# Kernel tuning notes

Measured on AMD Instinct MI355X. Metric: run time of the kernel, lower is better.

The kernel has to match this reference:

```python
import jax, jax.numpy as jnp
import numpy as np

N_NODES = 512
STATE_DIM = 32
MESSAGE_DIM = 32
H_MSG = 64
H_RO = 64
N_STEPS = 5


def setup_inputs() -> dict:
    key = jax.random.key(0)
    ks = jax.random.split(key, 20)
    s = 0.01  # torch init: normal(0, 0.01) weights, zero biases
    d, m = STATE_DIM, MESSAGE_DIM
    inp = {
        "J": jax.random.normal(ks[0], (N_NODES, N_NODES), jnp.float32),
        "b": jax.random.normal(ks[1], (N_NODES,), jnp.float32),
        # message-passing MLP
        "mp_W1": jax.random.normal(ks[2], (H_MSG, 2 * d + 3), jnp.float32) * s,
        "mp_b1": jnp.zeros((H_MSG,), jnp.float32),
        "mp_W2": jax.random.normal(ks[3], (H_MSG, H_MSG), jnp.float32) * s,
        "mp_b2": jnp.zeros((H_MSG,), jnp.float32),
        "mp_W3": jax.random.normal(ks[4], (m, H_MSG), jnp.float32) * s,
        "mp_b3": jnp.zeros((m,), jnp.float32),
        # GRU (input = state_dim + message_dim, hidden = state_dim); gate order r,z,n
        "gru_Wih": jax.random.normal(ks[5], (3 * d, d + m), jnp.float32) * 0.1,
        "gru_Whh": jax.random.normal(ks[6], (3 * d, d), jnp.float32) * 0.1,
        "gru_bih": jax.random.normal(ks[7], (3 * d,), jnp.float32) * 0.1,
        "gru_bhh": jax.random.normal(ks[8], (3 * d,), jnp.float32) * 0.1,
        # readout MLP
        "r_W1": jax.random.normal(ks[9], (H_RO, d), jnp.float32) * s,
        "r_b1": jnp.zeros((H_RO,), jnp.float32),
        "r_W2": jax.random.normal(ks[10], (H_RO, H_RO), jnp.float32) * s,
        "r_b2": jnp.zeros((H_RO,), jnp.float32),
        "r_W3": jax.random.normal(ks[11], (2, H_RO), jnp.float32) * s,
        "r_b3": jnp.zeros((2,), jnp.float32),
    }
    return inp


def reference(J, b, mp_W1, mp_b1, mp_W2, mp_b2, mp_W3, mp_b3,
              gru_Wih, gru_Whh, gru_bih, gru_bhh,
              r_W1, r_b1, r_W2, r_b2, r_W3, r_b3):
    n = J.shape[0]
    d = gru_Whh.shape[1]
    # split first message-layer weight by input segments to avoid building [n,n,2d+3]
    Wi, Wj = mp_W1[:, :d], mp_W1[:, d:2 * d]          # [H, d]
    wJ, wbi, wbj = mp_W1[:, 2 * d], mp_W1[:, 2 * d + 1], mp_W1[:, 2 * d + 2]  # [H]

    def step(h, _):
        # pre[i, j, :] = W1 @ cat(h_i, h_j, J_ij, b_i, b_j) + b1
        pre = ((h @ Wi.T)[:, None, :] + (h @ Wj.T)[None, :, :]
               + J[:, :, None] * wJ + b[:, None, None] * wbi
               + b[None, :, None] * wbj + mp_b1)          # [n, n, H]
        m1 = jax.nn.relu(pre)
        m2 = jax.nn.relu(m1 @ mp_W2.T + mp_b2)            # [n, n, H]
        msg = jax.nn.relu(m2 @ mp_W3.T + mp_b3)           # [n, n, M]
        msg_sum = msg.sum(axis=0)                         # sum over senders i -> [n, M]
        # GRU cell over all nodes (torch GRU, gate order r,z,n)
        x = jnp.concatenate([h, msg_sum], axis=-1)        # [n, d+M]
        gi = x @ gru_Wih.T + gru_bih                      # [n, 3d]
        gh = h @ gru_Whh.T + gru_bhh                      # [n, 3d]
        i_r, i_z, i_n = jnp.split(gi, 3, axis=-1)
        h_r, h_z, h_n = jnp.split(gh, 3, axis=-1)
        r = jax.nn.sigmoid(i_r + h_r)
        z = jax.nn.sigmoid(i_z + h_z)
        n_g = jnp.tanh(i_n + r * h_n)
        h_new = (1.0 - z) * n_g + z * h
        return h_new, None

    h0 = jnp.zeros((n, d), J.dtype)
    h, _ = jax.lax.scan(step, h0, None, length=N_STEPS)
    y = jax.nn.relu(h @ r_W1.T + r_b1)
    y = jax.nn.relu(y @ r_W2.T + r_b2)
    y = jax.nn.relu(y @ r_W3.T + r_b3)                    # [n, 2]
    return jax.nn.sigmoid(y)
```

## Files before the change

kernel.cpp:

```cpp
#include <hip/hip_runtime.h>
#include <math.h>

#define NN 512
#define SD 32
#define HM 64
#define NB 256
#define NGRP 16

typedef __bf16 bf16x8 __attribute__((ext_vector_type(8)));
typedef float floatx4 __attribute__((ext_vector_type(4)));

struct KParams {
    const float *J, *b, *mpW1, *mpb1, *mpW2, *mpb2, *mpW3, *mpb3;
    const float *Wih, *Whh, *bih, *bhh;
    const float *rW1, *rb1, *rW2, *rb2, *rW3, *rb3;
    float *out;
    float *hb0, *hb1;
    unsigned *bar;
};

__device__ __forceinline__ float sigmoidf_(float x) {
    return 1.0f / (1.0f + __expf(-x));
}

__device__ __forceinline__ unsigned ld_bypass_u32(const unsigned* p) {
    unsigned r;
    asm volatile("global_load_dword %0, %1, off sc0 sc1\n\ts_waitcnt vmcnt(0)"
                 : "=v"(r) : "v"(p) : "memory");
    return r;
}
__device__ __forceinline__ void issue4(const float* base,
        floatx4& a, floatx4& b, floatx4& c, floatx4& d) {
    asm volatile(
        "global_load_dwordx4 %0, %4, off sc0 sc1\n\t"
        "global_load_dwordx4 %1, %4, off offset:16 sc0 sc1\n\t"
        "global_load_dwordx4 %2, %4, off offset:128 sc0 sc1\n\t"
        "global_load_dwordx4 %3, %4, off offset:144 sc0 sc1"
        : "=&v"(a), "=&v"(b), "=&v"(c), "=&v"(d) : "v"(base));
}
__device__ __forceinline__ void wait4_8(floatx4& a, floatx4& b, floatx4& c, floatx4& d) {
    asm volatile("s_waitcnt vmcnt(8)" : "+v"(a), "+v"(b), "+v"(c), "+v"(d));
}
__device__ __forceinline__ void wait4_4(floatx4& a, floatx4& b, floatx4& c, floatx4& d) {
    asm volatile("s_waitcnt vmcnt(4)" : "+v"(a), "+v"(b), "+v"(c), "+v"(d));
}
__device__ __forceinline__ void wait4_0(floatx4& a, floatx4& b, floatx4& c, floatx4& d) {
    asm volatile("s_waitcnt vmcnt(0)" : "+v"(a), "+v"(b), "+v"(c), "+v"(d));
}

__device__ __forceinline__ void xbarrier(unsigned* bar, unsigned round, int bid) {
    __syncthreads();
    if (threadIdx.x == 0) {
        unsigned g = (unsigned)bid >> 4;
        unsigned old = atomicAdd(&bar[g * 16], 1u);
        if (old + 1u == round * NGRP) {
            unsigned r2 = atomicAdd(&bar[256], 1u);
            if (r2 + 1u == round * NGRP) {
                atomicMax(&bar[272], round);
            } else {
                while (ld_bypass_u32(&bar[272]) < round) __builtin_amdgcn_s_sleep(2);
            }
        } else {
            while (ld_bypass_u32(&bar[272]) < round) __builtin_amdgcn_s_sleep(2);
        }
    }
    __syncthreads();
}

__global__ __launch_bounds__(512, 2) void fused_kernel(KParams p)
{
    __shared__ __align__(16) float m2f[8][16][68];
    __shared__ float msum[8][32];
    __shared__ float hjpS[2][64];
    __shared__ float hS[2][32];
    __shared__ float msgS[2][32];
    __shared__ float giS[2][96], ghS[2][96];

    const int tid  = threadIdx.x;
    const int lane = tid & 63;
    const int wave = tid >> 6;
    const int nsel = wave >> 2;
    const int nw   = wave & 3;
    const int j    = blockIdx.x * 2 + nsel;
    const int q    = lane >> 4;
    const int c    = lane & 15;

    if (tid < 128) {
        int node = tid >> 6, cc = tid & 63;
        int jj = blockIdx.x * 2 + node;
        const float* wr = p.mpW1 + cc * 67;
        float bj = p.b[jj];
        hjpS[node][cc] = bj * wr[66] + p.mpb1[cc];
        atomicExch(&p.hb0[jj * HM + cc], bj * wr[65]);
    }

    float wj_r[16], b2v[4], b3v[2];
    #pragma unroll
    for (int s = 0; s < 8; ++s) {
        wj_r[s]     = p.mpW1[(q * 8 + s) * 67 + 64];
        wj_r[8 + s] = p.mpW1[(q * 8 + s + 32) * 67 + 64];
    }
    #pragma unroll
    for (int t4 = 0; t4 < 4; ++t4) b2v[t4] = p.mpb2[t4 * 16 + c];
    #pragma unroll
    for (int t2 = 0; t2 < 2; ++t2) b3v[t2] = p.mpb3[t2 * 16 + c];

    bf16x8 Bw2[2][4], Bw3[2][2];
    #pragma unroll
    for (int f = 0; f < 2; ++f)
        #pragma unroll
        for (int t4 = 0; t4 < 4; ++t4) {
            const float* src = p.mpW2 + (t4 * 16 + c) * 64 + f * 32 + q * 8;
            bf16x8 v;
            #pragma unroll
            for (int s = 0; s < 8; ++s) v[s] = (__bf16)src[s];
            Bw2[f][t4] = v;
        }
    #pragma unroll
    for (int f = 0; f < 2; ++f)
        #pragma unroll
        for (int t2 = 0; t2 < 2; ++t2) {
            const float* src = p.mpW3 + (t2 * 16 + c) * 64 + f * 32 + q * 8;
            bf16x8 v;
            #pragma unroll
            for (int s = 0; s < 8; ++s) v[s] = (__bf16)src[s];
            Bw3[f][t2] = v;
        }

    const float jA = p.J[(nw * 128 + lane) * NN + j];
    const float jB = p.J[(nw * 128 + 64 + lane) * NN + j];

    const floatx4 zero4 = {0.f, 0.f, 0.f, 0.f};

    xbarrier(p.bar, 1, blockIdx.x);

    for (int t = 0; t < 5; ++t) {
        const float* hb_read = (t & 1) ? p.hb1 : p.hb0;
        float*       hb_next = (t & 1) ? p.hb0 : p.hb1;

        float hjp_r[16];
        #pragma unroll
        for (int s = 0; s < 8; ++s) {
            hjp_r[s]     = hjpS[nsel][q * 8 + s];
            hjp_r[8 + s] = hjpS[nsel][q * 8 + s + 32];
        }
        float accf[2][4];
        #pragma unroll
        for (int t2 = 0; t2 < 2; ++t2)
            #pragma unroll
            for (int r = 0; r < 4; ++r) accf[t2][r] = 0.0f;

        floatx4 pf[3][4];
        issue4(hb_read + (nw * 128 + 0 * 16 + c) * 64 + q * 8,
               pf[0][0], pf[0][1], pf[0][2], pf[0][3]);
        issue4(hb_read + (nw * 128 + 1 * 16 + c) * 64 + q * 8,
               pf[1][0], pf[1][1], pf[1][2], pf[1][3]);

        #pragma unroll
        for (int g = 0; g < 8; ++g) {
            const int cur = g % 3;
            if (g < 6) {
                const int nxt = (g + 2) % 3;
                issue4(hb_read + (nw * 128 + (g + 2) * 16 + c) * 64 + q * 8,
                       pf[nxt][0], pf[nxt][1], pf[nxt][2], pf[nxt][3]);
                wait4_8(pf[cur][0], pf[cur][1], pf[cur][2], pf[cur][3]);
            } else if (g == 6) {
                wait4_4(pf[cur][0], pf[cur][1], pf[cur][2], pf[cur][3]);
            } else {
                wait4_0(pf[cur][0], pf[cur][1], pf[cur][2], pf[cur][3]);
            }
            floatx4 h0 = pf[cur][0], h1 = pf[cur][1];
            floatx4 h2 = pf[cur][2], h3 = pf[cur][3];

            float Jv = __shfl((g < 4) ? jA : jB, (g & 3) * 16 + c);

            float va[16];
            va[0]  = h0[0]; va[1]  = h0[1]; va[2]  = h0[2]; va[3]  = h0[3];
            va[4]  = h1[0]; va[5]  = h1[1]; va[6]  = h1[2]; va[7]  = h1[3];
            va[8]  = h2[0]; va[9]  = h2[1]; va[10] = h2[2]; va[11] = h2[3];
            va[12] = h3[0]; va[13] = h3[1]; va[14] = h3[2]; va[15] = h3[3];

            bf16x8 a0, a1;
            #pragma unroll
            for (int s = 0; s < 8; ++s) {
                float v0 = fmaf(Jv, wj_r[s],     va[s]     + hjp_r[s]);
                float v1 = fmaf(Jv, wj_r[8 + s], va[8 + s] + hjp_r[8 + s]);
                a0[s] = (__bf16)fmaxf(v0, 0.0f);
                a1[s] = (__bf16)fmaxf(v1, 0.0f);
            }

            floatx4 c1[4];
            #pragma unroll
            for (int t4 = 0; t4 < 4; ++t4) {
                c1[t4] = __builtin_amdgcn_mfma_f32_16x16x32_bf16(a0, Bw2[0][t4], zero4, 0, 0, 0);
                c1[t4] = __builtin_amdgcn_mfma_f32_16x16x32_bf16(a1, Bw2[1][t4], c1[t4], 0, 0, 0);
            }

            #pragma unroll
            for (int t4 = 0; t4 < 4; ++t4)
                #pragma unroll
                for (int r = 0; r < 4; ++r)
                    m2f[wave][q * 4 + r][t4 * 16 + c] = fmaxf(c1[t4][r] + b2v[t4], 0.0f);

            asm volatile("s_waitcnt lgkmcnt(0)" ::: "memory");

            float4 ra0 = *(const float4*)&m2f[wave][c][q * 8];
            float4 ra1 = *(const float4*)&m2f[wave][c][q * 8 + 4];
            float4 ra2 = *(const float4*)&m2f[wave][c][q * 8 + 32];
            float4 ra3 = *(const float4*)&m2f[wave][c][q * 8 + 36];

            bf16x8 a2, a3;
            a2[0] = (__bf16)ra0.x; a2[1] = (__bf16)ra0.y; a2[2] = (__bf16)ra0.z; a2[3] = (__bf16)ra0.w;
            a2[4] = (__bf16)ra1.x; a2[5] = (__bf16)ra1.y; a2[6] = (__bf16)ra1.z; a2[7] = (__bf16)ra1.w;
            a3[0] = (__bf16)ra2.x; a3[1] = (__bf16)ra2.y; a3[2] = (__bf16)ra2.z; a3[3] = (__bf16)ra2.w;
            a3[4] = (__bf16)ra3.x; a3[5] = (__bf16)ra3.y; a3[6] = (__bf16)ra3.z; a3[7] = (__bf16)ra3.w;

            floatx4 c2[2];
            #pragma unroll
            for (int t2 = 0; t2 < 2; ++t2) {
                c2[t2] = __builtin_amdgcn_mfma_f32_16x16x32_bf16(a2, Bw3[0][t2], zero4, 0, 0, 0);
                c2[t2] = __builtin_amdgcn_mfma_f32_16x16x32_bf16(a3, Bw3[1][t2], c2[t2], 0, 0, 0);
            }
            #pragma unroll
            for (int t2 = 0; t2 < 2; ++t2)
                #pragma unroll
                for (int r = 0; r < 4; ++r)
                    accf[t2][r] += fmaxf(c2[t2][r] + b3v[t2], 0.0f);

            asm volatile("s_waitcnt lgkmcnt(0)" ::: "memory");
        }

        float s0 = accf[0][0] + accf[0][1] + accf[0][2] + accf[0][3];
        float s1 = accf[1][0] + accf[1][1] + accf[1][2] + accf[1][3];
        s0 += __shfl_xor(s0, 16); s0 += __shfl_xor(s0, 32);
        s1 += __shfl_xor(s1, 16); s1 += __shfl_xor(s1, 32);
        if (lane < 16) {
            msum[wave][c]      = s0;
            msum[wave][16 + c] = s1;
        }
        __syncthreads();

        if (tid < 64) {
            int node = tid >> 5, d = tid & 31;
            msgS[node][d] = msum[node * 4 + 0][d] + msum[node * 4 + 1][d] +
                            msum[node * 4 + 2][d] + msum[node * 4 + 3][d];
        }
        __syncthreads();

        if (tid < 192) {
            int node = tid / 96, r = tid % 96;
            int g = r >> 5, d = r & 31;
            const float* wi = p.Wih + (g * 32 + d) * 64;
            float a  = p.bih[g * 32 + d];
            float bb = p.bhh[g * 32 + d];
            if (t > 0) {
                const float* wh = p.Whh + (g * 32 + d) * 32;
                #pragma unroll
                for (int k = 0; k < 32; ++k) {
                    float hv = hS[node][k];
                    a  = fmaf(hv, wi[k], a);
                    bb = fmaf(hv, wh[k], bb);
                }
            }
            #pragma unroll
            for (int k = 0; k < 32; ++k) a = fmaf(msgS[node][k], wi[32 + k], a);
            giS[node][r] = a; ghS[node][r] = bb;
        }
        __syncthreads();

        if (tid < 64) {
            int node = tid >> 5, d = tid & 31;
            float r  = sigmoidf_(giS[node][d] + ghS[node][d]);
            float z  = sigmoidf_(giS[node][32 + d] + ghS[node][32 + d]);
            float ng = tanhf(giS[node][64 + d] + r * ghS[node][64 + d]);
            float hold = (t > 0) ? hS[node][d] : 0.0f;
            hS[node][d] = (1.0f - z) * ng + z * hold;
        }
        __syncthreads();

        if (t < 4) {
            if (tid < 128) {
                int node = tid >> 6, cc = tid & 63;
                int jj = blockIdx.x * 2 + node;
                const float* wr = p.mpW1 + cc * 67;
                float bj = p.b[jj];
                float si = bj * wr[65];
                float sj = bj * wr[66] + p.mpb1[cc];
                #pragma unroll
                for (int d = 0; d < 32; ++d) {
                    float hv = hS[node][d];
                    si = fmaf(hv, wr[d], si);
                    sj = fmaf(hv, wr[32 + d], sj);
                }
                hjpS[node][cc] = sj;
                atomicExch(&hb_next[jj * HM + cc], si);
            }
            xbarrier(p.bar, (unsigned)(t + 2), blockIdx.x);
        } else {
            if (wave < 2) {
                int node = wave;
                int jj = blockIdx.x * 2 + node;
                float y1 = p.rb1[lane];
                #pragma unroll
                for (int k = 0; k < 32; ++k) y1 = fmaf(hS[node][k], p.rW1[lane * 32 + k], y1);
                y1 = fmaxf(y1, 0.0f);
                float y2 = p.rb2[lane];
                #pragma unroll
                for (int k = 0; k < 64; ++k) y2 = fmaf(__shfl(y1, k), p.rW2[lane * 64 + k], y2);
                y2 = fmaxf(y2, 0.0f);
                float y3 = (lane < 2) ? p.rb3[lane] : 0.0f;
                #pragma unroll
                for (int k = 0; k < 64; ++k) {
                    float v = __shfl(y2, k);
                    if (lane < 2) y3 = fmaf(v, p.rW3[lane * 64 + k], y3);
                }
                if (lane < 2) p.out[jj * 2 + lane] = sigmoidf_(y3);
            }
        }
    }
}

extern "C" void kernel_launch(void* const* d_in, const int* in_sizes, int n_in,
                              void* d_out, int out_size, void* d_ws, size_t ws_size,
                              hipStream_t stream)
{
    float* ws = (float*)d_ws;

    KParams p;
    p.J    = (const float*)d_in[0];
    p.b    = (const float*)d_in[1];
    p.mpW1 = (const float*)d_in[2];
    p.mpb1 = (const float*)d_in[3];
    p.mpW2 = (const float*)d_in[4];
    p.mpb2 = (const float*)d_in[5];
    p.mpW3 = (const float*)d_in[6];
    p.mpb3 = (const float*)d_in[7];
    p.Wih  = (const float*)d_in[8];
    p.Whh  = (const float*)d_in[9];
    p.bih  = (const float*)d_in[10];
    p.bhh  = (const float*)d_in[11];
    p.rW1  = (const float*)d_in[12];
    p.rb1  = (const float*)d_in[13];
    p.rW2  = (const float*)d_in[14];
    p.rb2  = (const float*)d_in[15];
    p.rW3  = (const float*)d_in[16];
    p.rb3  = (const float*)d_in[17];
    p.out  = (float*)d_out;

    p.hb0  = ws;
    p.hb1  = ws + 32768;
    p.bar  = (unsigned*)(ws + 65536);

    hipMemsetAsync(p.bar, 0, 4096, stream);

    fused_kernel<<<dim3(NB), dim3(512), 0, stream>>>(p);
}
```

Baseline: 183.0 us.

## Pack exchanged node projections as bf16 and stage them through LDS

The per-step exchanged sender projections are stored as packed bf16 pairs instead of fp32, halving global traffic. Each block now bulk-loads the whole projection table into a padded LDS buffer once per step instead of streaming it per wave with a prefetch pipeline. GRU weights and biases are also cached in padded LDS. This needs about 150KB of dynamic LDS, which limits occupancy to one block per CU and adds bf16 rounding of the projections.

```diff
diff --git a/kernel.cpp b/kernel.cpp
--- a/kernel.cpp
+++ b/kernel.cpp
@@ -9,13 +9,28 @@
 
 typedef __bf16 bf16x8 __attribute__((ext_vector_type(8)));
 typedef float floatx4 __attribute__((ext_vector_type(4)));
+typedef unsigned uintx4 __attribute__((ext_vector_type(4)));
+
+#define OFF_M2F   0
+#define OFF_HBS   34816
+#define OFF_WIH   112640
+#define OFF_WHH   137600
+#define OFF_BIH   150272
+#define OFF_BHH   150656
+#define OFF_MSUM  151040
+#define OFF_HJP   152064
+#define OFF_H     152576
+#define OFF_MSG   152832
+#define OFF_GI    153088
+#define OFF_GH    153856
+#define LDS_TOTAL 154624
 
 struct KParams {
     const float *J, *b, *mpW1, *mpb1, *mpW2, *mpb2, *mpW3, *mpb3;
     const float *Wih, *Whh, *bih, *bhh;
     const float *rW1, *rb1, *rW2, *rb2, *rW3, *rb3;
     float *out;
-    float *hb0, *hb1;
+    unsigned *hb0, *hb1;
     unsigned *bar;
 };
 
@@ -29,23 +44,18 @@
                  : "=v"(r) : "v"(p) : "memory");
     return r;
 }
-__device__ __forceinline__ void issue4(const float* base,
-        floatx4& a, floatx4& b, floatx4& c, floatx4& d) {
-    asm volatile(
-        "global_load_dwordx4 %0, %4, off sc0 sc1\n\t"
-        "global_load_dwordx4 %1, %4, off offset:16 sc0 sc1\n\t"
-        "global_load_dwordx4 %2, %4, off offset:128 sc0 sc1\n\t"
-        "global_load_dwordx4 %3, %4, off offset:144 sc0 sc1"
-        : "=&v"(a), "=&v"(b), "=&v"(c), "=&v"(d) : "v"(base));
-}
-__device__ __forceinline__ void wait4_8(floatx4& a, floatx4& b, floatx4& c, floatx4& d) {
-    asm volatile("s_waitcnt vmcnt(8)" : "+v"(a), "+v"(b), "+v"(c), "+v"(d));
-}
-__device__ __forceinline__ void wait4_4(floatx4& a, floatx4& b, floatx4& c, floatx4& d) {
-    asm volatile("s_waitcnt vmcnt(4)" : "+v"(a), "+v"(b), "+v"(c), "+v"(d));
-}
-__device__ __forceinline__ void wait4_0(floatx4& a, floatx4& b, floatx4& c, floatx4& d) {
-    asm volatile("s_waitcnt vmcnt(0)" : "+v"(a), "+v"(b), "+v"(c), "+v"(d));
+__device__ __forceinline__ void issue1(const unsigned* p, uintx4& d) {
+    asm volatile("global_load_dwordx4 %0, %1, off sc0 sc1"
+                 : "=v"(d) : "v"(p));
+}
+__device__ __forceinline__ void waitall8(uintx4* c) {
+    asm volatile("s_waitcnt vmcnt(0)"
+                 : "+v"(c[0]), "+v"(c[1]), "+v"(c[2]), "+v"(c[3]),
+                   "+v"(c[4]), "+v"(c[5]), "+v"(c[6]), "+v"(c[7]) :: "memory");
+}
+__device__ __forceinline__ void unpk(unsigned u, float& lo, float& hi) {
+    lo = __uint_as_float(u << 16);
+    hi = __uint_as_float(u & 0xffff0000u);
 }
 
 __device__ __forceinline__ void xbarrier(unsigned* bar, unsigned round, int bid) {
@@ -67,14 +77,21 @@
     __syncthreads();
 }
 
-__global__ __launch_bounds__(512, 2) void fused_kernel(KParams p)
+__global__ __launch_bounds__(512, 1) void fused_kernel(KParams p)
 {
-    __shared__ __align__(16) float m2f[8][16][68];
-    __shared__ float msum[8][32];
-    __shared__ float hjpS[2][64];
-    __shared__ float hS[2][32];
-    __shared__ float msgS[2][32];
-    __shared__ float giS[2][96], ghS[2][96];
+    extern __shared__ __align__(16) char smem[];
+    float (*m2f)[16][68] = (float(*)[16][68])(smem + OFF_M2F);
+    char*  hbS  = smem + OFF_HBS;
+    float* WihS = (float*)(smem + OFF_WIH);
+    float* WhhS = (float*)(smem + OFF_WHH);
+    float* biS  = (float*)(smem + OFF_BIH);
+    float* bhS  = (float*)(smem + OFF_BHH);
+    float (*msum)[32] = (float(*)[32])(smem + OFF_MSUM);
+    float (*hjpS)[64] = (float(*)[64])(smem + OFF_HJP);
+    float (*hS)[32]   = (float(*)[32])(smem + OFF_H);
+    float (*msgS)[32] = (float(*)[32])(smem + OFF_MSG);
+    float (*giS)[96]  = (float(*)[96])(smem + OFF_GI);
+    float (*ghS)[96]  = (float(*)[96])(smem + OFF_GH);
 
     const int tid  = threadIdx.x;
     const int lane = tid & 63;
@@ -85,13 +102,26 @@
     const int q    = lane >> 4;
     const int c    = lane & 15;
 
+    for (int n = tid; n < 96 * 64; n += 512)
+        WihS[(n >> 6) * 65 + (n & 63)] = p.Wih[n];
+    for (int n = tid; n < 96 * 32; n += 512)
+        WhhS[(n >> 5) * 33 + (n & 31)] = p.Whh[n];
+    if (tid < 96) biS[tid] = p.bih[tid];
+    else if (tid < 192) bhS[tid - 96] = p.bhh[tid - 96];
+
     if (tid < 128) {
         int node = tid >> 6, cc = tid & 63;
         int jj = blockIdx.x * 2 + node;
         const float* wr = p.mpW1 + cc * 67;
         float bj = p.b[jj];
         hjpS[node][cc] = bj * wr[66] + p.mpb1[cc];
-        atomicExch(&p.hb0[jj * HM + cc], bj * wr[65]);
+        float si = bj * wr[65];
+        float sp = __shfl(si, lane ^ 1);
+        if (!(lane & 1)) {
+            unsigned pk = (unsigned)__builtin_bit_cast(unsigned short, (__bf16)si)
+                        | ((unsigned)__builtin_bit_cast(unsigned short, (__bf16)sp) << 16);
+            atomicExch(&p.hb0[jj * 32 + (cc >> 1)], pk);
+        }
     }
 
     float wj_r[16], b2v[4], b3v[2];
@@ -135,8 +165,24 @@
     xbarrier(p.bar, 1, blockIdx.x);
 
     for (int t = 0; t < 5; ++t) {
-        const float* hb_read = (t & 1) ? p.hb1 : p.hb0;
-        float*       hb_next = (t & 1) ? p.hb0 : p.hb1;
+        const unsigned* hb_read = (t & 1) ? p.hb1 : p.hb0;
+        unsigned*       hb_next = (t & 1) ? p.hb0 : p.hb1;
+
+        {
+            uintx4 ck[8];
+            #pragma unroll
+            for (int k = 0; k < 8; ++k)
+                issue1(hb_read + (k * 512 + tid) * 4, ck[k]);
+            waitall8(ck);
+            #pragma unroll
+            for (int k = 0; k < 8; ++k) {
+                int n = k * 512 + tid;
+                char* dst = hbS + (n >> 3) * 152 + (n & 7) * 16;
+                *(uint2*)dst       = make_uint2(ck[k][0], ck[k][1]);
+                *(uint2*)(dst + 8) = make_uint2(ck[k][2], ck[k][3]);
+            }
+        }
+        __syncthreads();
 
         float hjp_r[16];
         #pragma unroll
@@ -150,41 +196,27 @@
             #pragma unroll
             for (int r = 0; r < 4; ++r) accf[t2][r] = 0.0f;
 
-        floatx4 pf[3][4];
-        issue4(hb_read + (nw * 128 + 0 * 16 + c) * 64 + q * 8,
-               pf[0][0], pf[0][1], pf[0][2], pf[0][3]);
-        issue4(hb_read + (nw * 128 + 1 * 16 + c) * 64 + q * 8,
-               pf[1][0], pf[1][1], pf[1][2], pf[1][3]);
-
         #pragma unroll
         for (int g = 0; g < 8; ++g) {
-            const int cur = g % 3;
-            if (g < 6) {
-                const int nxt = (g + 2) % 3;
-                issue4(hb_read + (nw * 128 + (g + 2) * 16 + c) * 64 + q * 8,
-                       pf[nxt][0], pf[nxt][1], pf[nxt][2], pf[nxt][3]);
-                wait4_8(pf[cur][0], pf[cur][1], pf[cur][2], pf[cur][3]);
-            } else if (g == 6) {
-                wait4_4(pf[cur][0], pf[cur][1], pf[cur][2], pf[cur][3]);
-            } else {
-                wait4_0(pf[cur][0], pf[cur][1], pf[cur][2], pf[cur][3]);
-            }
-            floatx4 h0 = pf[cur][0], h1 = pf[cur][1];
-            floatx4 h2 = pf[cur][2], h3 = pf[cur][3];
+            const char* rb = hbS + (nw * 128 + g * 16 + c) * 152;
+            uint2 u0 = *(const uint2*)(rb + q * 16);
+            uint2 u1 = *(const uint2*)(rb + q * 16 + 8);
+            uint2 u2 = *(const uint2*)(rb + 64 + q * 16);
+            uint2 u3 = *(const uint2*)(rb + 64 + q * 16 + 8);
 
             float Jv = __shfl((g < 4) ? jA : jB, (g & 3) * 16 + c);
 
-            float va[16];
-            va[0]  = h0[0]; va[1]  = h0[1]; va[2]  = h0[2]; va[3]  = h0[3];
-            va[4]  = h1[0]; va[5]  = h1[1]; va[6]  = h1[2]; va[7]  = h1[3];
-            va[8]  = h2[0]; va[9]  = h2[1]; va[10] = h2[2]; va[11] = h2[3];
-            va[12] = h3[0]; va[13] = h3[1]; va[14] = h3[2]; va[15] = h3[3];
+            float f[16];
+            unpk(u0.x, f[0],  f[1]);  unpk(u0.y, f[2],  f[3]);
+            unpk(u1.x, f[4],  f[5]);  unpk(u1.y, f[6],  f[7]);
+            unpk(u2.x, f[8],  f[9]);  unpk(u2.y, f[10], f[11]);
+            unpk(u3.x, f[12], f[13]); unpk(u3.y, f[14], f[15]);
 
             bf16x8 a0, a1;
             #pragma unroll
             for (int s = 0; s < 8; ++s) {
-                float v0 = fmaf(Jv, wj_r[s],     va[s]     + hjp_r[s]);
-                float v1 = fmaf(Jv, wj_r[8 + s], va[8 + s] + hjp_r[8 + s]);
+                float v0 = fmaf(Jv, wj_r[s],     f[s]     + hjp_r[s]);
+                float v1 = fmaf(Jv, wj_r[8 + s], f[8 + s] + hjp_r[8 + s]);
                 a0[s] = (__bf16)fmaxf(v0, 0.0f);
                 a1[s] = (__bf16)fmaxf(v1, 0.0f);
             }
@@ -250,11 +282,11 @@
         if (tid < 192) {
             int node = tid / 96, r = tid % 96;
             int g = r >> 5, d = r & 31;
-            const float* wi = p.Wih + (g * 32 + d) * 64;
-            float a  = p.bih[g * 32 + d];
-            float bb = p.bhh[g * 32 + d];
+            const float* wi = WihS + (g * 32 + d) * 65;
+            const float* wh = WhhS + (g * 32 + d) * 33;
+            float a  = biS[g * 32 + d];
+            float bb = bhS[g * 32 + d];
             if (t > 0) {
-                const float* wh = p.Whh + (g * 32 + d) * 32;
                 #pragma unroll
                 for (int k = 0; k < 32; ++k) {
                     float hv = hS[node][k];
@@ -293,7 +325,12 @@
                     sj = fmaf(hv, wr[32 + d], sj);
                 }
                 hjpS[node][cc] = sj;
-                atomicExch(&hb_next[jj * HM + cc], si);
+                float sp = __shfl(si, lane ^ 1);
+                if (!(lane & 1)) {
+                    unsigned pk = (unsigned)__builtin_bit_cast(unsigned short, (__bf16)si)
+                                | ((unsigned)__builtin_bit_cast(unsigned short, (__bf16)sp) << 16);
+                    atomicExch(&hb_next[jj * 32 + (cc >> 1)], pk);
+                }
             }
             xbarrier(p.bar, (unsigned)(t + 2), blockIdx.x);
         } else {
@@ -347,11 +384,13 @@
     p.rb3  = (const float*)d_in[17];
     p.out  = (float*)d_out;
 
-    p.hb0  = ws;
-    p.hb1  = ws + 32768;
-    p.bar  = (unsigned*)(ws + 65536);
+    p.hb0  = (unsigned*)ws;
+    p.hb1  = (unsigned*)(ws + 16384);
+    p.bar  = (unsigned*)(ws + 32768);
 
     hipMemsetAsync(p.bar, 0, 4096, stream);
 
-    fused_kernel<<<dim3(NB), dim3(512), 0, stream>>>(p);
-}
+    hipFuncSetAttribute((const void*)fused_kernel,
+                        hipFuncAttributeMaxDynamicSharedMemorySize, LDS_TOTAL);
+    fused_kernel<<<dim3(NB), dim3(512), LDS_TOTAL, stream>>>(p);
+}
```

Result: faster. 177.5 us (-3.0%).
